# Optimization experiments

Hardware: AMD Instinct MI355X
Metric: run time of the kernel (lower is better)

The kernel has to match this reference:

```python
import jax, jax.numpy as jnp
import numpy as np

K = 27  # num_neighs, hardcoded in module
EPS = 1e-5


def knn_idx(x, k):
    # x: (B, N, 3) -> (B, N, k) indices of k nearest neighbors (self included)
    xx = jnp.sum(x * x, axis=-1)                      # (B, N)
    inner = jnp.einsum('bnd,bmd->bnm', x, x)          # (B, N, N)
    d = 2.0 * inner - xx[:, :, None] - xx[:, None, :] # negative sq dist
    return jax.lax.top_k(d, k)[1]


def graph_feature(f, idx):
    # f: (B, N, C), idx: (B, N, k) -> (B, N, k, 2C) = [neigh - center, center]
    neigh = jax.vmap(lambda fb, ib: fb[ib])(f, idx)   # (B, N, k, C)
    center = jnp.broadcast_to(f[:, :, None, :], neigh.shape)
    return jnp.concatenate([neigh - center, center], axis=-1)


def bn_lrelu(y, g, b, axes):
    m = jnp.mean(y, axis=axes, keepdims=True)
    v = jnp.var(y, axis=axes, keepdims=True)
    y = (y - m) * jax.lax.rsqrt(v + EPS) * g + b
    return jnp.where(y >= 0, y, 0.2 * y)


def edge_conv(f, idx, W, g, b):
    # f: (B, N, C) -> (B, N, C_out); 1x1 conv over (B, 2C, N, k) + BN + LeakyReLU + max over k
    h = graph_feature(f, idx)                         # (B, N, k, 2C)
    y = jnp.einsum('bnkc,oc->bnko', h, W)             # (B, N, k, C_out)
    y = bn_lrelu(y, g, b, axes=(0, 1, 2))
    return jnp.max(y, axis=2)                         # (B, N, C_out)


def setup_inputs() -> dict:
    key = jax.random.key(0)
    ks = jax.random.split(key, 8)
    B, N, latent = 2, 2048, 256
    x = jax.random.normal(ks[0], (B, N, 3), dtype=jnp.float32)
    chans = [(6, 96), (192, 192), (384, 384), (768, 768)]
    inp = {'x': x}
    for i, (cin, cout) in enumerate(chans):
        inp[f'W{i}'] = jax.random.normal(ks[1 + i], (cout, cin), dtype=jnp.float32) * np.sqrt(2.0 / cin).astype(np.float32)
        inp[f'g{i}'] = jnp.ones((cout,), dtype=jnp.float32)
        inp[f'b{i}'] = jnp.zeros((cout,), dtype=jnp.float32)
    inp['W4'] = jax.random.normal(ks[5], (latent, 1440), dtype=jnp.float32) * np.sqrt(2.0 / 1440).astype(np.float32)
    inp['g4'] = jnp.ones((latent,), dtype=jnp.float32)
    inp['b4'] = jnp.zeros((latent,), dtype=jnp.float32)
    return inp


def reference(x, W0, g0, b0, W1, g1, b1, W2, g2, b2, W3, g3, b3, W4, g4, b4):
    # x: (B, N, 3)
    idx = knn_idx(x, K)                               # (B, N, K), fixed for all layers (only_true_neighs=True)
    outs = []
    f = x
    for (W, g, b) in ((W0, g0, b0), (W1, g1, b1), (W2, g2, b2), (W3, g3, b3)):
        f = edge_conv(f, idx, W, g, b)
        outs.append(f)
    h = jnp.concatenate(outs, axis=-1)                # (B, N, 1440)
    y = jnp.einsum('bnc,oc->bno', h, W4)              # (B, N, latent)
    feats = bn_lrelu(y, g4, b4, axes=(0, 1))          # features_per_point (B, N, latent)
    global_feat = jnp.max(feats, axis=1)              # (B, latent)
    return global_feat, feats
```

## Files before the change

kernel.cpp:

```cpp
#include <hip/hip_runtime.h>
#include <hip/hip_bf16.h>

#define BATCH 2
#define NPB   2048
#define NPTS  4096
#define KNB   27
#define FCATC 1440
#define CSTRIDE 1696
#define NSLOT 32
#define PBATCH 4

#define WOFF_L1 0
#define WOFF_L2 36864
#define WOFF_L3 184320
#define WOFF_F  774144
#define WTOTAL  1142784

typedef __hip_bfloat16 bf16;
typedef __attribute__((ext_vector_type(8))) short short8;
typedef __attribute__((ext_vector_type(4))) float f32x4;
typedef __attribute__((ext_vector_type(2))) short s16x2;

__device__ __forceinline__ float b2f(bf16 v) { return __bfloat162float(v); }

__device__ __forceinline__ void split_bf16(float v, bf16& h, bf16& l) {
    h = __float2bfloat16(v);
    l = __float2bfloat16(v - b2f(h));
}

__device__ __forceinline__ float ldin(const void* p, size_t i, int f32) {
    return f32 ? ((const float*)p)[i] : b2f(((const bf16*)p)[i]);
}

__global__ void k_init(const void* __restrict__ x, int* __restrict__ flag,
                       float* __restrict__ xf, float* __restrict__ slots) {
    if (blockIdx.x < 424) {
        slots[blockIdx.x * 256 + threadIdx.x] = 0.f;
        return;
    }
    __shared__ int s;
    if (threadIdx.x == 0) s = 0;
    __syncthreads();
    const bf16* xb = (const bf16*)x;
    int local = 0;
    for (int i = threadIdx.x; i < NPTS * 3; i += 256) {
        float v = b2f(xb[i]);
        if (!(fabsf(v) < 1e4f)) local = 1;
    }
    if (local) s = 1;
    __syncthreads();
    int f32 = s;
    if (threadIdx.x == 0) flag[0] = f32;
    for (int i = threadIdx.x; i < NPTS * 3; i += 256) xf[i] = ldin(x, i, f32);
}

__global__ __launch_bounds__(256) void k_knn(const float* __restrict__ x, int* __restrict__ idx) {
    __shared__ uint hist4[4][260];
    __shared__ uint hist[256];
    __shared__ uint tkey[NPB];
    __shared__ int  tix[NPB];
    __shared__ uint s_phigh;
    __shared__ int  s_rem, s_outcnt, s_tiecnt;

    int bn = blockIdx.x, b = bn >> 11, n = bn & (NPB - 1);
    int tid = threadIdx.x;
    int wv = tid >> 6;
    const float* xb = x + (size_t)b * NPB * 3;
    float cx = xb[n * 3 + 0], cy = xb[n * 3 + 1], cz = xb[n * 3 + 2];
    float cc = cx * cx + cy * cy + cz * cz;

    uint u[8];
    #pragma unroll
    for (int j = 0; j < 8; j++) {
        int m = j * 256 + tid;
        float mx = xb[m * 3 + 0], my = xb[m * 3 + 1], mz = xb[m * 3 + 2];
        float d = 2.f * (cx * mx + cy * my + cz * mz) - cc - (mx * mx + my * my + mz * mz);
        uint s = __float_as_uint(d);
        u[j] = (s & 0x80000000u) ? ~s : (s | 0x80000000u);
    }
    if (tid == 0) { s_phigh = 0; s_rem = KNB; s_outcnt = 0; s_tiecnt = 0; }

    for (int pass = 0; pass < 2; pass++) {
        int shift = 24 - pass * 8;
        hist[tid] = 0;
        for (int i = tid; i < 4 * 260; i += 256) ((uint*)hist4)[i] = 0;
        __syncthreads();
        uint phigh = s_phigh;
        #pragma unroll
        for (int j = 0; j < 8; j++) {
            bool in = (pass == 0) || ((u[j] >> (shift + 8)) == phigh);
            if (in) atomicAdd(&hist4[wv][(u[j] >> shift) & 0xFFu], 1u);
        }
        __syncthreads();
        hist[tid] = hist4[0][tid] + hist4[1][tid] + hist4[2][tid] + hist4[3][tid];
        __syncthreads();
        if (tid < 64) {
            int L = tid;
            uint c0 = hist[L * 4 + 0], c1 = hist[L * 4 + 1], c2 = hist[L * 4 + 2], c3 = hist[L * 4 + 3];
            uint s = c0 + c1 + c2 + c3;
            uint acc = s;
            #pragma unroll
            for (int off = 1; off < 64; off <<= 1) {
                uint t = __shfl_down(acc, off);
                if (L + off < 64) acc += t;
            }
            uint excl = acc - s;
            int rem = s_rem;
            if ((int)excl < rem && (int)acc >= rem) {
                uint cs[4] = { c0, c1, c2, c3 };
                uint cum = excl;
                int bsel = 0; uint hb = 0;
                #pragma unroll
                for (int q = 3; q >= 0; q--) {
                    if ((int)cum < rem && (int)(cum + cs[q]) >= rem && hb == 0u && bsel == 0) {
                        bsel = L * 4 + q; hb = cs[q]; cum += cs[q];
                    } else if (bsel == 0 && hb == 0u) {
                        cum += cs[q];
                    }
                }
                int strictlyAbove = (int)(cum - hb);
                s_rem = rem - strictlyAbove;
                s_phigh = (phigh << 8) | (uint)bsel;
            }
        }
        __syncthreads();
    }

    uint T16 = s_phigh;
    #pragma unroll
    for (int j = 0; j < 8; j++) {
        int m = j * 256 + tid;
        uint hi = u[j] >> 16;
        if (hi > T16) {
            int p = atomicAdd(&s_outcnt, 1);
            idx[bn * KNB + p] = b * NPB + m;
        } else if (hi == T16) {
            int p = atomicAdd(&s_tiecnt, 1);
            tkey[p] = u[j];
            tix[p] = m;
        }
    }
    __syncthreads();
    int outcnt = s_outcnt, rem = s_rem, tiecnt = s_tiecnt;
    if (tiecnt == rem) {
        if (tid < rem) idx[bn * KNB + outcnt + tid] = b * NPB + tix[tid];
    } else if (tid == 0) {
        for (int t = 0; t < rem; t++) {
            int bi = 0;
            for (int q = 1; q < tiecnt; q++)
                if (tkey[q] > tkey[bi] || (tkey[q] == tkey[bi] && tix[q] < tix[bi])) bi = q;
            idx[bn * KNB + outcnt + t] = b * NPB + tix[bi];
            tkey[bi] = 0; tix[bi] = 0x7fffffff;
        }
    }
}

__global__ void k_l0(const float* __restrict__ xf, const void* __restrict__ W,
                     const int* __restrict__ flag, bf16* __restrict__ Ub, float* __restrict__ Vf) {
    int i = blockIdx.x * 256 + threadIdx.x;
    if (i >= NPTS * 192) return;
    int bn = i / 192, o = i % 192;
    int f32 = flag[0];
    float x0 = xf[bn * 3 + 0], x1 = xf[bn * 3 + 1], x2 = xf[bn * 3 + 2];
    if (o < 96) {
        float r = x0 * ldin(W, o * 6 + 0, f32) + x1 * ldin(W, o * 6 + 1, f32) + x2 * ldin(W, o * 6 + 2, f32);
        Ub[(size_t)bn * 96 + o] = __float2bfloat16(r);
    } else {
        int oo = o - 96;
        float w0 = ldin(W, oo * 6 + 3, f32) - ldin(W, oo * 6 + 0, f32);
        float w1 = ldin(W, oo * 6 + 4, f32) - ldin(W, oo * 6 + 1, f32);
        float w2 = ldin(W, oo * 6 + 5, f32) - ldin(W, oo * 6 + 2, f32);
        Vf[(size_t)bn * 96 + oo] = x0 * w0 + x1 * w1 + x2 * w2;
    }
}

__global__ void k_wt_all(const void* __restrict__ W1, const void* __restrict__ W2,
                         const void* __restrict__ W3, const void* __restrict__ W4,
                         const int* __restrict__ flag,
                         bf16* __restrict__ Wh, bf16* __restrict__ Wl) {
    int i = blockIdx.x * 256 + threadIdx.x;
    if (i >= WTOTAL) return;
    int f32 = flag[0];
    float w;
    if (i < WOFF_L2) {
        int row = i / 96, c = i % 96;
        w = (row < 192) ? ldin(W1, (size_t)row * 192 + c, f32)
                        : ldin(W1, (size_t)(row - 192) * 192 + 96 + c, f32)
                          - ldin(W1, (size_t)(row - 192) * 192 + c, f32);
    } else if (i < WOFF_L3) {
        int j = i - WOFF_L2;
        int row = j / 192, c = j % 192;
        w = (row < 384) ? ldin(W2, (size_t)row * 384 + c, f32)
                        : ldin(W2, (size_t)(row - 384) * 384 + 192 + c, f32)
                          - ldin(W2, (size_t)(row - 384) * 384 + c, f32);
    } else if (i < WOFF_F) {
        int j = i - WOFF_L3;
        int row = j / 384, c = j % 384;
        w = (row < 768) ? ldin(W3, (size_t)row * 768 + c, f32)
                        : ldin(W3, (size_t)(row - 768) * 768 + 384 + c, f32)
                          - ldin(W3, (size_t)(row - 768) * 768 + c, f32);
    } else {
        int j = i - WOFF_F;
        w = ldin(W4, j, f32);
    }
    bf16 h, l; split_bf16(w, h, l);
    Wh[i] = h; Wl[i] = l;
}

__global__ __launch_bounds__(256) void k_gemm_mfma(const bf16* __restrict__ Ah, const bf16* __restrict__ Al,
                                                   int lda, int aoff,
                                                   const bf16* __restrict__ Bh, const bf16* __restrict__ Bl,
                                                   int K, bf16* __restrict__ Cu, float* __restrict__ Cv,
                                                   int Cosplit, int ldc, int ksz, int zstride) {
    __shared__ bf16 Ash[64][40];
    __shared__ bf16 Asl[64][40];
    __shared__ bf16 Bsh[64][40];
    __shared__ bf16 Bsl[64][40];
    int tid = threadIdx.x;
    int wave = tid >> 6, lane = tid & 63;
    int wm = wave >> 1, wn = wave & 1;
    int quad = lane >> 4, l15 = lane & 15;
    int Lxy = blockIdx.y * gridDim.x + blockIdx.x;
    int stripe = Lxy & 7;
    int w = Lxy >> 3;
    int mb = stripe * 8 + (w & 7);
    int nb = w >> 3;
    int m0 = mb * 64, n0 = nb * 64;
    int kbase = blockIdx.z * ksz;
    float* Cz = Cv + (size_t)blockIdx.z * zstride;
    int lr = tid >> 2, lc = (tid & 3) * 8;

    f32x4 acc[2][2] = {};
    for (int k0 = kbase; k0 < kbase + ksz; k0 += 32) {
        size_t ao = (size_t)(m0 + lr) * lda + aoff + k0 + lc;
        size_t bo = (size_t)(n0 + lr) * K + k0 + lc;
        *(short8*)&Ash[lr][lc] = *(const short8*)&Ah[ao];
        *(short8*)&Asl[lr][lc] = *(const short8*)&Al[ao];
        *(short8*)&Bsh[lr][lc] = *(const short8*)&Bh[bo];
        *(short8*)&Bsl[lr][lc] = *(const short8*)&Bl[bo];
        __syncthreads();
        short8 ah0 = *(const short8*)&Ash[wm * 32 + l15][quad * 8];
        short8 ah1 = *(const short8*)&Ash[wm * 32 + 16 + l15][quad * 8];
        short8 al0 = *(const short8*)&Asl[wm * 32 + l15][quad * 8];
        short8 al1 = *(const short8*)&Asl[wm * 32 + 16 + l15][quad * 8];
        short8 bh0 = *(const short8*)&Bsh[wn * 32 + l15][quad * 8];
        short8 bh1 = *(const short8*)&Bsh[wn * 32 + 16 + l15][quad * 8];
        short8 bl0 = *(const short8*)&Bsl[wn * 32 + l15][quad * 8];
        short8 bl1 = *(const short8*)&Bsl[wn * 32 + 16 + l15][quad * 8];
        acc[0][0] = __builtin_amdgcn_mfma_f32_16x16x32_bf16(ah0, bl0, acc[0][0], 0, 0, 0);
        acc[0][0] = __builtin_amdgcn_mfma_f32_16x16x32_bf16(al0, bh0, acc[0][0], 0, 0, 0);
        acc[0][0] = __builtin_amdgcn_mfma_f32_16x16x32_bf16(ah0, bh0, acc[0][0], 0, 0, 0);
        acc[0][1] = __builtin_amdgcn_mfma_f32_16x16x32_bf16(ah0, bl1, acc[0][1], 0, 0, 0);
        acc[0][1] = __builtin_amdgcn_mfma_f32_16x16x32_bf16(al0, bh1, acc[0][1], 0, 0, 0);
        acc[0][1] = __builtin_amdgcn_mfma_f32_16x16x32_bf16(ah0, bh1, acc[0][1], 0, 0, 0);
        acc[1][0] = __builtin_amdgcn_mfma_f32_16x16x32_bf16(ah1, bl0, acc[1][0], 0, 0, 0);
        acc[1][0] = __builtin_amdgcn_mfma_f32_16x16x32_bf16(al1, bh0, acc[1][0], 0, 0, 0);
        acc[1][0] = __builtin_amdgcn_mfma_f32_16x16x32_bf16(ah1, bh0, acc[1][0], 0, 0, 0);
        acc[1][1] = __builtin_amdgcn_mfma_f32_16x16x32_bf16(ah1, bl1, acc[1][1], 0, 0, 0);
        acc[1][1] = __builtin_amdgcn_mfma_f32_16x16x32_bf16(al1, bh1, acc[1][1], 0, 0, 0);
        acc[1][1] = __builtin_amdgcn_mfma_f32_16x16x32_bf16(ah1, bh1, acc[1][1], 0, 0, 0);
        __syncthreads();
    }
    #pragma unroll
    for (int mt = 0; mt < 2; mt++) {
        #pragma unroll
        for (int nt = 0; nt < 2; nt++) {
            int col = n0 + wn * 32 + nt * 16 + l15;
            #pragma unroll
            for (int i = 0; i < 4; i++) {
                int row = m0 + wm * 32 + mt * 16 + quad * 4 + i;
                if (Cosplit > 0) {
                    if (col < Cosplit) Cu[(size_t)row * Cosplit + col] = __float2bfloat16(acc[mt][nt][i]);
                    else               Cv[(size_t)row * Cosplit + col - Cosplit] = acc[mt][nt][i];
                } else {
                    Cz[(size_t)row * ldc + col] = acc[mt][nt][i];
                }
            }
        }
    }
}

__global__ __launch_bounds__(256) void k_gather(const bf16* __restrict__ Ub, float* __restrict__ Vf,
                                                const int* __restrict__ idx,
                                                bf16* __restrict__ fch, bf16* __restrict__ fcl,
                                                float* __restrict__ ssum, float* __restrict__ ssq,
                                                int Co, int out_off) {
    __shared__ int srow[PBATCH * KNB];
    int tid = threadIdx.x;
    int L = blockIdx.y * gridDim.x + blockIdx.x;
    int batch = L & 1;
    int w = L >> 1;
    int pg = batch * 512 + (w & 511);
    int chunk = w >> 9;
    int p0 = pg * PBATCH;
    if (tid < PBATCH * KNB) srow[tid] = idx[p0 * KNB + tid] * Co;
    __syncthreads();
    int P = Co >> 1;
    int op = chunk * 256 + tid;
    if (op >= P) return;
    int o = op * 2;
    int slot = pg & (NSLOT - 1);
    float s0 = 0.f, s1 = 0.f, q0 = 0.f, q1 = 0.f;
    #pragma unroll 1
    for (int p = 0; p < PBATCH; p++) {
        int bn = p0 + p;
        float2 vv = *(const float2*)&Vf[(size_t)bn * Co + o];
        float ymax0 = -INFINITY, ymax1 = -INFINITY, ymin0 = INFINITY, ymin1 = INFINITY;
        #pragma unroll
        for (int k = 0; k < KNB; k++) {
            uint wb = *(const uint*)&Ub[(size_t)srow[p * KNB + k] + o];
            float y0 = __uint_as_float(wb << 16) + vv.x;
            float y1 = __uint_as_float(wb & 0xffff0000u) + vv.y;
            ymax0 = fmaxf(ymax0, y0); ymin0 = fminf(ymin0, y0); s0 += y0; q0 += y0 * y0;
            ymax1 = fmaxf(ymax1, y1); ymin1 = fminf(ymin1, y1); s1 += y1; q1 += y1 * y1;
        }
        size_t fi = (size_t)bn * FCATC + out_off + o;
        bf16 hh[2], ll[2];
        split_bf16(ymax0, hh[0], ll[0]);
        split_bf16(ymax1, hh[1], ll[1]);
        *(s16x2*)&fch[fi] = *(const s16x2*)hh;
        *(s16x2*)&fcl[fi] = *(const s16x2*)ll;
        *(float2*)&Vf[(size_t)bn * Co + o] = make_float2(ymin0, ymin1);
    }
    atomicAdd(&ssum[slot * CSTRIDE + o + 0], s0);
    atomicAdd(&ssum[slot * CSTRIDE + o + 1], s1);
    atomicAdd(&ssq [slot * CSTRIDE + o + 0], q0);
    atomicAdd(&ssq [slot * CSTRIDE + o + 1], q1);
}

__global__ void k_scaleshift(const float* __restrict__ ssum, const float* __restrict__ ssq,
                             const void* __restrict__ g, const void* __restrict__ bb,
                             const int* __restrict__ flag,
                             float* __restrict__ scale, float* __restrict__ shift, int Co, float invcnt) {
    int o = blockIdx.x * 256 + threadIdx.x;
    if (o >= Co) return;
    int f32 = flag[0];
    float s = 0.f, q = 0.f;
    for (int c = 0; c < NSLOT; c++) { s += ssum[c * CSTRIDE + o]; q += ssq[c * CSTRIDE + o]; }
    float mean = s * invcnt;
    float var = q * invcnt - mean * mean;
    float sc = ldin(g, o, f32) * rsqrtf(var + 1e-5f);
    scale[o] = sc;
    shift[o] = ldin(bb, o, f32) - mean * sc;
}

__global__ __launch_bounds__(256) void k_apply(const float* __restrict__ Vf,
                                               const float* __restrict__ scale, const float* __restrict__ shift,
                                               bf16* __restrict__ fch, bf16* __restrict__ fcl,
                                               int Co, int out_off) {
    int bn = blockIdx.x;
    for (int o = threadIdx.x; o < Co; o += 256) {
        float sc = scale[o], sh = shift[o];
        size_t fi = (size_t)bn * FCATC + out_off + o;
        float y = (sc >= 0.f) ? (b2f(fch[fi]) + b2f(fcl[fi]))
                              : Vf[(size_t)bn * Co + o];
        float z = sc * y + sh;
        z = (z >= 0.f) ? z : 0.2f * z;
        bf16 h, l; split_bf16(z, h, l);
        fch[fi] = h; fcl[fi] = l;
    }
}

__global__ void k_stats_final(const float* __restrict__ part, float* __restrict__ Y,
                              float* __restrict__ ssum, float* __restrict__ ssq) {
    int o = threadIdx.x;
    int p0 = blockIdx.x * 128;
    const size_t PL = (size_t)NPTS * 256;
    float s = 0, q = 0;
    for (int p = 0; p < 128; p++) {
        size_t i = (size_t)(p0 + p) * 256 + o;
        float y = part[i] + part[i + PL] + part[i + 2 * PL] + part[i + 3 * PL] + part[i + 4 * PL];
        Y[i] = y;
        s += y; q += y * y;
    }
    ssum[blockIdx.x * CSTRIDE + o] = s;
    ssq [blockIdx.x * CSTRIDE + o] = q;
}

__global__ void k_feats(const float* __restrict__ Y, const float* __restrict__ ssum,
                        const float* __restrict__ ssq, const void* __restrict__ g,
                        const void* __restrict__ bb, const int* __restrict__ flag,
                        void* __restrict__ out, float* __restrict__ partial) {
    int o = threadIdx.x;
    int chunk = blockIdx.x;
    int bn0 = chunk * 64;
    int f32 = flag[0];
    float s = 0.f, q = 0.f;
    for (int c = 0; c < NSLOT; c++) { s += ssum[c * CSTRIDE + o]; q += ssq[c * CSTRIDE + o]; }
    float mean = s * (1.f / (float)NPTS);
    float var = q * (1.f / (float)NPTS) - mean * mean;
    float sc = ldin(g, o, f32) * rsqrtf(var + 1e-5f);
    float sh = ldin(bb, o, f32) - mean * sc;
    float best = -INFINITY;
    for (int i = 0; i < 64; i++) {
        int bn = bn0 + i;
        float z = sc * Y[(size_t)bn * 256 + o] + sh;
        z = (z >= 0.f) ? z : 0.2f * z;
        size_t oi = (size_t)BATCH * 256 + (size_t)bn * 256 + o;
        if (f32) ((float*)out)[oi] = z;
        else     ((bf16*)out)[oi] = __float2bfloat16(z);
        best = fmaxf(best, z);
    }
    partial[chunk * 256 + o] = best;
}

__global__ void k_gmax(const float* __restrict__ partial, void* __restrict__ out, const int* __restrict__ flag) {
    int o = threadIdx.x;
    int b = blockIdx.x;
    float best = -INFINITY;
    for (int c = 0; c < 32; c++) best = fmaxf(best, partial[(b * 32 + c) * 256 + o]);
    if (flag[0]) ((float*)out)[b * 256 + o] = best;
    else         ((bf16*)out)[b * 256 + o] = __float2bfloat16(best);
}

extern "C" void kernel_launch(void* const* d_in, const int* in_sizes, int n_in,
                              void* d_out, int out_size, void* d_ws, size_t ws_size,
                              hipStream_t stream) {
    const void* x = d_in[0];

    char* ws = (char*)d_ws;
    int*   idx    = (int*)  (ws + 0);
    bf16*  Ub     = (bf16*) (ws + 442368);
    float* Vf     = (float*)(ws + 6733824);
    float* part   = (float*)(ws + 442368);
    bf16*  fch    = (bf16*) (ws + 25608192);
    bf16*  fcl    = (bf16*) (ws + 37404672);
    float* Y4     = (float*)(ws + 49201152);
    bf16*  Whall  = (bf16*) (ws + 53395456);
    bf16*  Wlall  = (bf16*) (ws + 55681024);
    float* slots  = (float*)(ws + 57966592);
    float* ssum   = slots;
    float* ssq    = slots + NSLOT * CSTRIDE;
    float* scales = (float*)(ws + 58400768);
    float* shifts = (float*)(ws + 58407552);
    float* partial= (float*)(ws + 58414336);
    float* xf     = (float*)(ws + 58479872);
    int*   flag   = (int*)  (ws + 58529024);

    const int Cin[4]  = {3, 96, 192, 384};
    const int Co[4]   = {96, 192, 384, 768};
    const int ooff[4] = {0, 96, 288, 672};
    const int soff[5] = {0, 96, 288, 672, 1440};
    const int woff[4] = {0, WOFF_L1, WOFF_L2, WOFF_L3};

    hipLaunchKernelGGL(k_init, dim3(425), dim3(256), 0, stream, x, flag, xf, slots);
    hipLaunchKernelGGL(k_knn, dim3(NPTS), dim3(256), 0, stream, xf, idx);
    hipLaunchKernelGGL(k_wt_all, dim3((WTOTAL + 255) / 256), dim3(256), 0, stream,
                       d_in[4], d_in[7], d_in[10], d_in[13], flag, Whall, Wlall);

    const float invcnt_edge = 1.f / (float)(NPTS * KNB);
    for (int L = 0; L < 4; L++) {
        const void* g  = d_in[2 + 3 * L];
        const void* bb = d_in[3 + 3 * L];
        int N2 = 2 * Co[L];
        if (L == 0) {
            hipLaunchKernelGGL(k_l0, dim3((NPTS * 192 + 255) / 256), dim3(256), 0, stream,
                               xf, d_in[1], flag, Ub, Vf);
        } else {
            hipLaunchKernelGGL(k_gemm_mfma, dim3(N2 / 64, NPTS / 64, 1), dim3(256), 0, stream,
                               fch, fcl, FCATC, ooff[L - 1], Whall + woff[L], Wlall + woff[L], Cin[L],
                               Ub, Vf, Co[L], 0, Cin[L], 0);
        }
        int nchunks = ((Co[L] / 2) + 255) / 256;
        hipLaunchKernelGGL(k_gather, dim3(NPTS / PBATCH, nchunks), dim3(256), 0, stream,
                           Ub, Vf, idx, fch, fcl, ssum + soff[L], ssq + soff[L], Co[L], ooff[L]);
        hipLaunchKernelGGL(k_scaleshift, dim3((Co[L] + 255) / 256), dim3(256), 0, stream,
                           ssum + soff[L], ssq + soff[L], g, bb, flag,
                           scales + soff[L], shifts + soff[L], Co[L], invcnt_edge);
        hipLaunchKernelGGL(k_apply, dim3(NPTS), dim3(256), 0, stream,
                           Vf, scales + soff[L], shifts + soff[L], fch, fcl, Co[L], ooff[L]);
    }

    hipLaunchKernelGGL(k_gemm_mfma, dim3(256 / 64, NPTS / 64, 5), dim3(256), 0, stream,
                       fch, fcl, FCATC, 0, Whall + WOFF_F, Wlall + WOFF_F, FCATC,
                       (bf16*)nullptr, part, 0, 256, 288, NPTS * 256);
    hipLaunchKernelGGL(k_stats_final, dim3(32), dim3(256), 0, stream, part, Y4, ssum + soff[4], ssq + soff[4]);
    hipLaunchKernelGGL(k_feats, dim3(64), dim3(256), 0, stream, Y4, ssum + soff[4], ssq + soff[4],
                       d_in[14], d_in[15], flag, d_out, partial);
    hipLaunchKernelGGL(k_gmax, dim3(BATCH), dim3(256), 0, stream, partial, d_out, flag);
}
```

Before: 340.5 us.

## Enlarge MFMA GEMM tiles to 128x128 and load tiles via direct global-to-LDS

The split-bf16 GEMM now computes 128x128 output tiles per block, with each wave holding a 4x4 set of 16x16 accumulators, up from 64x64 tiles with 2x2 per wave. Tile loads use the global_load_lds builtin to copy directly into shared memory without passing through registers. Fragments are read into registers before the second barrier so the MFMAs run after it. This raises operand reuse and cuts load instruction overhead, but it quarters the grid size, which may underfill the GPU for the smaller layers. It also drops the LDS row padding, which can cause bank conflicts on fragment reads.

```diff
diff --git a/kernel.cpp b/kernel.cpp
--- a/kernel.cpp
+++ b/kernel.cpp
@@ -30,6 +30,13 @@
 
 __device__ __forceinline__ float ldin(const void* p, size_t i, int f32) {
     return f32 ? ((const float*)p)[i] : b2f(((const bf16*)p)[i]);
+}
+
+__device__ __forceinline__ void gl16(const bf16* g, bf16* l) {
+    __builtin_amdgcn_global_load_lds(
+        (const __attribute__((address_space(1))) unsigned int*)g,
+        (__attribute__((address_space(3))) unsigned int*)l,
+        16, 0, 0);
 }
 
 __global__ void k_init(const void* __restrict__ x, int* __restrict__ flag,
@@ -212,10 +219,10 @@
                                                    const bf16* __restrict__ Bh, const bf16* __restrict__ Bl,
                                                    int K, bf16* __restrict__ Cu, float* __restrict__ Cv,
                                                    int Cosplit, int ldc, int ksz, int zstride) {
-    __shared__ bf16 Ash[64][40];
-    __shared__ bf16 Asl[64][40];
-    __shared__ bf16 Bsh[64][40];
-    __shared__ bf16 Bsl[64][40];
+    __shared__ __align__(16) bf16 Ash[128][32];
+    __shared__ __align__(16) bf16 Asl[128][32];
+    __shared__ __align__(16) bf16 Bsh[128][32];
+    __shared__ __align__(16) bf16 Bsl[128][32];
     int tid = threadIdx.x;
     int wave = tid >> 6, lane = tid & 63;
     int wm = wave >> 1, wn = wave & 1;
@@ -223,52 +230,68 @@
     int Lxy = blockIdx.y * gridDim.x + blockIdx.x;
     int stripe = Lxy & 7;
     int w = Lxy >> 3;
-    int mb = stripe * 8 + (w & 7);
-    int nb = w >> 3;
-    int m0 = mb * 64, n0 = nb * 64;
+    int mb = stripe * 4 + (w & 3);
+    int nb = w >> 2;
+    int m0 = mb * 128, n0 = nb * 128;
     int kbase = blockIdx.z * ksz;
     float* Cz = Cv + (size_t)blockIdx.z * zstride;
-    int lr = tid >> 2, lc = (tid & 3) * 8;
-
-    f32x4 acc[2][2] = {};
+
+    int c0 = wave * 64 + lane;
+    int c1 = c0 + 256;
+    int ar0 = c0 >> 2, ac0 = (c0 & 3) << 3;
+    int ar1 = c1 >> 2, ac1 = (c1 & 3) << 3;
+    size_t aRow0 = (size_t)(m0 + ar0) * lda + aoff;
+    size_t aRow1 = (size_t)(m0 + ar1) * lda + aoff;
+    size_t bRow0 = (size_t)(n0 + ar0) * K;
+    size_t bRow1 = (size_t)(n0 + ar1) * K;
+    bf16* sA  = &Ash[0][0] + wave * 512;
+    bf16* sAl = &Asl[0][0] + wave * 512;
+    bf16* sB  = &Bsh[0][0] + wave * 512;
+    bf16* sBl = &Bsl[0][0] + wave * 512;
+
+    f32x4 acc[4][4] = {};
     for (int k0 = kbase; k0 < kbase + ksz; k0 += 32) {
-        size_t ao = (size_t)(m0 + lr) * lda + aoff + k0 + lc;
-        size_t bo = (size_t)(n0 + lr) * K + k0 + lc;
-        *(short8*)&Ash[lr][lc] = *(const short8*)&Ah[ao];
-        *(short8*)&Asl[lr][lc] = *(const short8*)&Al[ao];
-        *(short8*)&Bsh[lr][lc] = *(const short8*)&Bh[bo];
-        *(short8*)&Bsl[lr][lc] = *(const short8*)&Bl[bo];
+        gl16(Ah + aRow0 + k0 + ac0, sA);
+        gl16(Ah + aRow1 + k0 + ac1, sA + 2048);
+        gl16(Al + aRow0 + k0 + ac0, sAl);
+        gl16(Al + aRow1 + k0 + ac1, sAl + 2048);
+        gl16(Bh + bRow0 + k0 + ac0, sB);
+        gl16(Bh + bRow1 + k0 + ac1, sB + 2048);
+        gl16(Bl + bRow0 + k0 + ac0, sBl);
+        gl16(Bl + bRow1 + k0 + ac1, sBl + 2048);
         __syncthreads();
-        short8 ah0 = *(const short8*)&Ash[wm * 32 + l15][quad * 8];
-        short8 ah1 = *(const short8*)&Ash[wm * 32 + 16 + l15][quad * 8];
-        short8 al0 = *(const short8*)&Asl[wm * 32 + l15][quad * 8];
-        short8 al1 = *(const short8*)&Asl[wm * 32 + 16 + l15][quad * 8];
-        short8 bh0 = *(const short8*)&Bsh[wn * 32 + l15][quad * 8];
-        short8 bh1 = *(const short8*)&Bsh[wn * 32 + 16 + l15][quad * 8];
-        short8 bl0 = *(const short8*)&Bsl[wn * 32 + l15][quad * 8];
-        short8 bl1 = *(const short8*)&Bsl[wn * 32 + 16 + l15][quad * 8];
-        acc[0][0] = __builtin_amdgcn_mfma_f32_16x16x32_bf16(ah0, bl0, acc[0][0], 0, 0, 0);
-        acc[0][0] = __builtin_amdgcn_mfma_f32_16x16x32_bf16(al0, bh0, acc[0][0], 0, 0, 0);
-        acc[0][0] = __builtin_amdgcn_mfma_f32_16x16x32_bf16(ah0, bh0, acc[0][0], 0, 0, 0);
-        acc[0][1] = __builtin_amdgcn_mfma_f32_16x16x32_bf16(ah0, bl1, acc[0][1], 0, 0, 0);
-        acc[0][1] = __builtin_amdgcn_mfma_f32_16x16x32_bf16(al0, bh1, acc[0][1], 0, 0, 0);
-        acc[0][1] = __builtin_amdgcn_mfma_f32_16x16x32_bf16(ah0, bh1, acc[0][1], 0, 0, 0);
-        acc[1][0] = __builtin_amdgcn_mfma_f32_16x16x32_bf16(ah1, bl0, acc[1][0], 0, 0, 0);
-        acc[1][0] = __builtin_amdgcn_mfma_f32_16x16x32_bf16(al1, bh0, acc[1][0], 0, 0, 0);
-        acc[1][0] = __builtin_amdgcn_mfma_f32_16x16x32_bf16(ah1, bh0, acc[1][0], 0, 0, 0);
-        acc[1][1] = __builtin_amdgcn_mfma_f32_16x16x32_bf16(ah1, bl1, acc[1][1], 0, 0, 0);
-        acc[1][1] = __builtin_amdgcn_mfma_f32_16x16x32_bf16(al1, bh1, acc[1][1], 0, 0, 0);
-        acc[1][1] = __builtin_amdgcn_mfma_f32_16x16x32_bf16(ah1, bh1, acc[1][1], 0, 0, 0);
+        short8 ahf[4], alf[4], bhf[4], blf[4];
+        #pragma unroll
+        for (int mt = 0; mt < 4; mt++) {
+            int rr = wm * 64 + mt * 16 + l15;
+            ahf[mt] = *(const short8*)&Ash[rr][quad * 8];
+            alf[mt] = *(const short8*)&Asl[rr][quad * 8];
+        }
+        #pragma unroll
+        for (int nt = 0; nt < 4; nt++) {
+            int rr = wn * 64 + nt * 16 + l15;
+            bhf[nt] = *(const short8*)&Bsh[rr][quad * 8];
+            blf[nt] = *(const short8*)&Bsl[rr][quad * 8];
+        }
         __syncthreads();
+        #pragma unroll
+        for (int mt = 0; mt < 4; mt++) {
+            #pragma unroll
+            for (int nt = 0; nt < 4; nt++) {
+                acc[mt][nt] = __builtin_amdgcn_mfma_f32_16x16x32_bf16(ahf[mt], blf[nt], acc[mt][nt], 0, 0, 0);
+                acc[mt][nt] = __builtin_amdgcn_mfma_f32_16x16x32_bf16(alf[mt], bhf[nt], acc[mt][nt], 0, 0, 0);
+                acc[mt][nt] = __builtin_amdgcn_mfma_f32_16x16x32_bf16(ahf[mt], bhf[nt], acc[mt][nt], 0, 0, 0);
+            }
+        }
     }
     #pragma unroll
-    for (int mt = 0; mt < 2; mt++) {
+    for (int mt = 0; mt < 4; mt++) {
         #pragma unroll
-        for (int nt = 0; nt < 2; nt++) {
-            int col = n0 + wn * 32 + nt * 16 + l15;
+        for (int nt = 0; nt < 4; nt++) {
+            int col = n0 + wn * 64 + nt * 16 + l15;
             #pragma unroll
             for (int i = 0; i < 4; i++) {
-                int row = m0 + wm * 32 + mt * 16 + quad * 4 + i;
+                int row = m0 + wm * 64 + mt * 16 + quad * 4 + i;
                 if (Cosplit > 0) {
                     if (col < Cosplit) Cu[(size_t)row * Cosplit + col] = __float2bfloat16(acc[mt][nt][i]);
                     else               Cv[(size_t)row * Cosplit + col - Cosplit] = acc[mt][nt][i];
@@ -457,7 +480,7 @@
             hipLaunchKernelGGL(k_l0, dim3((NPTS * 192 + 255) / 256), dim3(256), 0, stream,
                                xf, d_in[1], flag, Ub, Vf);
         } else {
-            hipLaunchKernelGGL(k_gemm_mfma, dim3(N2 / 64, NPTS / 64, 1), dim3(256), 0, stream,
+            hipLaunchKernelGGL(k_gemm_mfma, dim3(N2 / 128, NPTS / 128, 1), dim3(256), 0, stream,
                                fch, fcl, FCATC, ooff[L - 1], Whall + woff[L], Wlall + woff[L], Cin[L],
                                Ub, Vf, Co[L], 0, Cin[L], 0);
         }
@@ -471,7 +494,7 @@
                            Vf, scales + soff[L], shifts + soff[L], fch, fcl, Co[L], ooff[L]);
     }
 
-    hipLaunchKernelGGL(k_gemm_mfma, dim3(256 / 64, NPTS / 64, 5), dim3(256), 0, stream,
+    hipLaunchKernelGGL(k_gemm_mfma, dim3(256 / 128, NPTS / 128, 5), dim3(256), 0, stream,
                        fch, fcl, FCATC, 0, Whall + WOFF_F, Wlall + WOFF_F, FCATC,
                        (bf16*)nullptr, part, 0, 256, 288, NPTS * 256);
     hipLaunchKernelGGL(k_stats_final, dim3(32), dim3(256), 0, stream, part, Y4, ssum + soff[4], ssq + soff[4]);
```

Result: slower. 351.4 us (+3.2%).
